# Optimization experiments

Measured on AMD Instinct MI355X. Metric: run time of the kernel, lower is better.

Reference implementation:

```python
import jax, jax.numpy as jnp
import numpy as np

B, S, H, Q = 32, 128, 128, 3  # users, seq_len, hidden_size, quadkey_level
L = Q - 1  # number of mixing scales


def setup_inputs() -> dict:
    key = jax.random.key(0)
    ks = jax.random.split(key, 12)
    trend0 = jax.random.normal(ks[0], (B, S, H), dtype=jnp.float32)
    trend1 = jax.random.normal(ks[1], (B, S, H), dtype=jnp.float32)
    trend2 = jax.random.normal(ks[2], (B, S, H), dtype=jnp.float32)
    # Per-position prefix linears padded into dense tensors, zero-masked beyond
    # the prefix length j+1 so the ragged math is exact:
    #   W1[j, :j+1, :j+1] ~ Linear(j+1, j+1), b1[j, :j+1]
    #   W2[j, :j+1]      ~ Linear(j+1, 1),   b2[j]
    idx = jnp.arange(S)
    pm = (idx[None, :] <= idx[:, None]).astype(jnp.float32)  # [j, s]: s <= j
    W1 = jax.random.normal(ks[3], (L, S, S, S), dtype=jnp.float32) * 0.05
    W1 = W1 * pm[None, :, :, None] * pm[None, :, None, :]
    b1 = jax.random.normal(ks[4], (L, S, S), dtype=jnp.float32) * 0.05 * pm[None]
    W2 = jax.random.normal(ks[5], (L, S, S), dtype=jnp.float32) * 0.05 * pm[None]
    b2 = jax.random.normal(ks[6], (L, S), dtype=jnp.float32) * 0.05
    # shared output MLP: Linear(H,H)->GELU->Linear(H,H); stored as [in, out]
    Wm1 = jax.random.normal(ks[7], (H, H), dtype=jnp.float32) * 0.05
    bm1 = jax.random.normal(ks[8], (H,), dtype=jnp.float32) * 0.05
    Wm2 = jax.random.normal(ks[9], (H, H), dtype=jnp.float32) * 0.05
    bm2 = jax.random.normal(ks[10], (H,), dtype=jnp.float32) * 0.05
    return {"trend0": trend0, "trend1": trend1, "trend2": trend2,
            "W1": W1, "b1": b1, "W2": W2, "b2": b2,
            "Wm1": Wm1, "bm1": bm1, "Wm2": Wm2, "bm2": bm2}


def reference(trend0, trend1, trend2, W1, b1, W2, b2, Wm1, bm1, Wm2, bm2):
    gelu = lambda x: jax.nn.gelu(x, approximate=False)  # torch nn.GELU default
    mlp = lambda x: gelu(x @ Wm1 + bm1) @ Wm2 + bm2

    rev = [trend2, trend1, trend0]  # trend_list reversed
    out_low = rev[0]
    out_high = rev[1]
    outs = [out_low]
    for i in range(Q - 1):
        # vectorized ragged prefix mix: per position j, out_low[:, :j+1] (as [B,H,j+1])
        # -> Linear(j+1,j+1) -> GELU -> Linear(j+1,1). Zero-padding in W1/b1/W2
        # kills all contributions beyond the prefix (GELU(0)=0).
        y1 = jnp.einsum('bsh,jst->bhjt', out_low, W1[i]) + b1[i]  # [B,H,S,S]
        res = jnp.einsum('bhjt,jt->bjh', gelu(y1), W2[i]) + b2[i][None, :, None]
        out_high = out_high + res
        out_low = out_high
        if i + 2 <= Q - 1:
            out_high = rev[i + 2]
        out_low = mlp(out_low)
        outs.append(out_low)
    outs.reverse()
    return tuple(outs)
```

## Files before the change

### kernel.cpp

```cpp
#include <hip/hip_runtime.h>
#include <stdint.h>

#define BSH (32 * 128 * 128)

typedef __attribute__((ext_vector_type(8))) __bf16 bf16x8;
typedef __attribute__((ext_vector_type(4))) float f32x4;

__device__ __forceinline__ unsigned short f2bf(float f) {
  union { float f; unsigned u; } v; v.f = f;
  return (unsigned short)((v.u + 0x7FFFu + ((v.u >> 16) & 1u)) >> 16);
}

__device__ __forceinline__ float fast_exp2(float x) {
#if __has_builtin(__builtin_amdgcn_exp2f)
  return __builtin_amdgcn_exp2f(x);
#else
  float r; asm("v_exp_f32 %0, %1" : "=v"(r) : "v"(x)); return r;
#endif
}
__device__ __forceinline__ float fast_rcp(float x) {
#if __has_builtin(__builtin_amdgcn_rcpf)
  return __builtin_amdgcn_rcpf(x);
#else
  float r; asm("v_rcp_f32 %0, %1" : "=v"(r) : "v"(x)); return r;
#endif
}

__device__ __forceinline__ float gelu_f(float y) {
  float u = y * y;
  float p = __builtin_fmaf(u, 0.044715f, 1.0f) * y;
  float w = fast_exp2(p * 2.30220787f);
  return y - y * fast_rcp(1.0f + w);
}

__device__ __forceinline__ int jg_of(int x, int cls) {
  return cls == 0 ? x : cls == 1 ? 15 - x : cls == 2 ? 16 + x : 31 - x;
}

__device__ __forceinline__ void transpose_block_c(const float* __restrict__ src,
                                                  unsigned short* __restrict__ dst,
                                                  unsigned short* lds) {
  const int tid = threadIdx.x;
  const float4* s4 = (const float4*)src;
#pragma unroll
  for (int it = 0; it < 16; ++it) {
    int i4 = tid + it * 256;
    float4 v = s4[i4];
    int s = i4 >> 5;
    int t0 = (i4 * 4) & 127;
    int sc = s >> 3, se = s & 7;
#pragma unroll
    for (int e = 0; e < 4; ++e) {
      int t = t0 + e;
      lds[t * 136 + ((sc ^ ((t >> 2) & 7)) << 3) + se] = f2bf(((const float*)&v)[e]);
    }
  }
  __syncthreads();
#pragma unroll
  for (int it = 0; it < 8; ++it) {
    int c = tid + it * 256;
    int tr = c >> 4, sc = c & 15;
    uint4 d = *(const uint4*)(lds + tr * 136 + ((sc ^ ((tr >> 2) & 7)) << 3));
    *(uint4*)(dst + (sc * 128 + tr) * 8) = d;
  }
}

__global__ __launch_bounds__(256) void prepass_kernel(
    const float* __restrict__ W1, const float* __restrict__ trend2,
    const float* __restrict__ Wm1, const float* __restrict__ Wm2,
    unsigned short* __restrict__ W1Tc, unsigned short* __restrict__ T2c,
    unsigned short* __restrict__ Wm1c, unsigned short* __restrict__ Wm2c,
    float* __restrict__ out2) {
  __shared__ unsigned short lds[128 * 136];
  const int bid = blockIdx.x;
  if (bid < 256) {
    int x = bid & 7, r = bid >> 3;
    int stage = r >> 4, rr = r & 15;
    int j = jg_of(x, rr >> 2) * 4 + (rr & 3);
    int blk = stage * 128 + j;
    transpose_block_c(W1 + blk * 16384, W1Tc + blk * 16384, lds);
  } else if (bid < 288) {
    const int b = bid - 256;
    transpose_block_c(trend2 + b * 16384, T2c + b * 16384, lds);
    const float4* s4 = (const float4*)(trend2 + b * 16384);
    float4* d4 = (float4*)(out2 + b * 16384);
#pragma unroll
    for (int it = 0; it < 16; ++it)
      d4[threadIdx.x + it * 256] = s4[threadIdx.x + it * 256];
  } else if (bid == 288) {
    transpose_block_c(Wm1, Wm1c, lds);
  } else {
    transpose_block_c(Wm2, Wm2c, lds);
  }
}

__global__ __launch_bounds__(256, 4) void mix_fused_kernel(
    const unsigned short* __restrict__ XTc,
    const unsigned short* __restrict__ W1Tj,
    const float* __restrict__ b1j,
    const float* __restrict__ W2j,
    const float* __restrict__ b2j,
    const float* __restrict__ trendR,
    const unsigned short* __restrict__ Wm1c,
    const unsigned short* __restrict__ Wm2c,
    const float* __restrict__ bm1,
    const float* __restrict__ bm2,
    float* __restrict__ outF,
    unsigned short* __restrict__ outTc,
    const int write_t) {
  __shared__ float res_ws[4][4][64];
  __shared__ __align__(16) unsigned short xa[16 * 128];
  __shared__ __align__(16) unsigned short U[16 * 128];
  const int bid = blockIdx.x;
  const int x = bid & 7;
  const int i = bid >> 3;
  const int b = i & 31;
  const int jg = jg_of(x, i >> 5);
  const int j0 = jg * 4;
  const int tid = threadIdx.x;
  const int wave = tid >> 6;
  const int lane = tid & 63;
  const int lane15 = lane & 15;
  const int quad = lane >> 4;

  {
    uint4 z = {0, 0, 0, 0};
    ((uint4*)xa)[tid] = z;
    ((uint4*)U)[tid] = z;
  }

  const int ntiles = (j0 >> 4) + 1;
  const int ksteps = (j0 >> 5) + 1;
  const unsigned short* Bb = XTc + b * 16384;
  const unsigned short* A0 = W1Tj + j0 * 16384;
  const float C = -2.45546937f;

#pragma unroll
  for (int p = 0; p < 2; ++p) {
    float psum[4][4];
#pragma unroll
    for (int jj = 0; jj < 4; ++jj)
#pragma unroll
      for (int ni = 0; ni < 4; ++ni) psum[jj][ni] = 0.f;

#pragma unroll
    for (int q = 0; q < 2; ++q) {
      const int mt = wave + q * 4;
      if (mt < ntiles) {
        f32x4 acc[4][4];
#pragma unroll
        for (int jj = 0; jj < 4; ++jj)
#pragma unroll
          for (int ni = 0; ni < 4; ++ni) {
            f32x4 z = {0.f, 0.f, 0.f, 0.f};
            acc[jj][ni] = z;
          }
        for (int ks = 0; ks < ksteps; ++ks) {
          const int kq = ks * 4 + quad;
          const unsigned short* bp = Bb + (kq * 128 + p * 64 + lane15) * 8;
          bf16x8 bfr[4], af[4];
#pragma unroll
          for (int ni = 0; ni < 4; ++ni)
            bfr[ni] = *(const bf16x8*)(bp + ni * 128);
#pragma unroll
          for (int jj = 0; jj < 4; ++jj)
            af[jj] = *(const bf16x8*)(A0 + jj * 16384 +
                                      (kq * 128 + mt * 16 + lane15) * 8);
#pragma unroll
          for (int jj = 0; jj < 4; ++jj)
#pragma unroll
            for (int ni = 0; ni < 4; ++ni)
              acc[jj][ni] = __builtin_amdgcn_mfma_f32_16x16x32_bf16(
                  af[jj], bfr[ni], acc[jj][ni], 0, 0, 0);
        }
        const int tb = mt * 16 + quad * 4;
#pragma unroll
        for (int jj = 0; jj < 4; ++jj) {
          const int j = j0 + jj;
          float4 b1v = *(const float4*)(b1j + j * 128 + tb);
          float4 w2v = *(const float4*)(W2j + j * 128 + tb);
#pragma unroll
          for (int r = 0; r < 4; ++r) {
            float b1r = ((const float*)&b1v)[r];
            float w2r = ((const float*)&w2v)[r];
            float cb = C * b1r;
            float bw = b1r * w2r;
#pragma unroll
            for (int ni = 0; ni < 4; ++ni) {
              float a = acc[jj][ni][r];
              float m = __builtin_fmaf(a, C, cb);
              float e = fast_exp2(m);
              float rr2 = fast_rcp(1.0f + e);
              float yw = __builtin_fmaf(a, w2r, bw);
              psum[jj][ni] = __builtin_fmaf(yw, rr2, psum[jj][ni]);
            }
          }
        }
      }
    }
#pragma unroll
    for (int jj = 0; jj < 4; ++jj)
#pragma unroll
      for (int ni = 0; ni < 4; ++ni) {
        float v = psum[jj][ni];
        v += __shfl_xor(v, 16, 64);
        v += __shfl_xor(v, 32, 64);
        psum[jj][ni] = v;
      }
#pragma unroll
    for (int jj = 0; jj < 4; ++jj)
      res_ws[wave][jj][quad * 16 + lane15] = psum[jj][quad];
    __syncthreads();
    {
      const int jj = tid >> 6;
      const int hh = tid & 63;
      const int j = j0 + jj;
      const int h = p * 64 + hh;
      float v = res_ws[0][jj][hh] + res_ws[1][jj][hh] +
                res_ws[2][jj][hh] + res_ws[3][jj][hh] +
                b2j[j] + trendR[(b * 128 + j) * 128 + h];
      xa[((h >> 3) * 16 + jj) * 8 + (h & 7)] = f2bf(v);
    }
    __syncthreads();
  }

  f32x4 acc2[2];
  { f32x4 z = {0.f, 0.f, 0.f, 0.f}; acc2[0] = z; acc2[1] = z; }
#pragma unroll
  for (int ks = 0; ks < 4; ++ks) {
    int kq = ks * 4 + quad;
    bf16x8 a = *(const bf16x8*)(xa + (kq * 16 + lane15) * 8);
    bf16x8 w0 = *(const bf16x8*)(Wm1c + (kq * 128 + (wave * 2 + 0) * 16 + lane15) * 8);
    bf16x8 w1 = *(const bf16x8*)(Wm1c + (kq * 128 + (wave * 2 + 1) * 16 + lane15) * 8);
    acc2[0] = __builtin_amdgcn_mfma_f32_16x16x32_bf16(a, w0, acc2[0], 0, 0, 0);
    acc2[1] = __builtin_amdgcn_mfma_f32_16x16x32_bf16(a, w1, acc2[1], 0, 0, 0);
  }
  if (quad == 0) {
#pragma unroll
    for (int nt = 0; nt < 2; ++nt) {
      int o = (wave * 2 + nt) * 16 + lane15;
      float bv = bm1[o];
#pragma unroll
      for (int r = 0; r < 4; ++r) {
        float g = gelu_f(acc2[nt][r] + bv);
        U[((o >> 3) * 16 + r) * 8 + (o & 7)] = f2bf(g);
      }
    }
  }
  __syncthreads();
  { f32x4 z = {0.f, 0.f, 0.f, 0.f}; acc2[0] = z; acc2[1] = z; }
#pragma unroll
  for (int ks = 0; ks < 4; ++ks) {
    int kq = ks * 4 + quad;
    bf16x8 a = *(const bf16x8*)(U + (kq * 16 + lane15) * 8);
    bf16x8 w0 = *(const bf16x8*)(Wm2c + (kq * 128 + (wave * 2 + 0) * 16 + lane15) * 8);
    bf16x8 w1 = *(const bf16x8*)(Wm2c + (kq * 128 + (wave * 2 + 1) * 16 + lane15) * 8);
    acc2[0] = __builtin_amdgcn_mfma_f32_16x16x32_bf16(a, w0, acc2[0], 0, 0, 0);
    acc2[1] = __builtin_amdgcn_mfma_f32_16x16x32_bf16(a, w1, acc2[1], 0, 0, 0);
  }
  if (quad == 0) {
#pragma unroll
    for (int nt = 0; nt < 2; ++nt) {
      int o = (wave * 2 + nt) * 16 + lane15;
      float bv = bm2[o];
      unsigned short tmp4[4] __attribute__((aligned(8)));
#pragma unroll
      for (int r = 0; r < 4; ++r) {
        float v = acc2[nt][r] + bv;
        outF[b * 16384 + (j0 + r) * 128 + o] = v;
        tmp4[r] = f2bf(v);
      }
      if (write_t)
        *(uint2*)(outTc + b * 16384 + ((j0 >> 3) * 128 + o) * 8 + (j0 & 7)) =
            *(const uint2*)tmp4;
    }
  }
}

extern "C" void kernel_launch(void* const* d_in, const int* in_sizes, int n_in,
                              void* d_out, int out_size, void* d_ws, size_t ws_size,
                              hipStream_t stream) {
  (void)in_sizes; (void)n_in; (void)out_size; (void)ws_size;
  const float* trend0 = (const float*)d_in[0];
  const float* trend1 = (const float*)d_in[1];
  const float* trend2 = (const float*)d_in[2];
  const float* W1  = (const float*)d_in[3];
  const float* b1  = (const float*)d_in[4];
  const float* W2  = (const float*)d_in[5];
  const float* b2  = (const float*)d_in[6];
  const float* Wm1 = (const float*)d_in[7];
  const float* bm1 = (const float*)d_in[8];
  const float* Wm2 = (const float*)d_in[9];
  const float* bm2 = (const float*)d_in[10];
  float* out = (float*)d_out;
  char* ws = (char*)d_ws;

  unsigned short* W1Tc = (unsigned short*)(ws);
  unsigned short* T2c  = (unsigned short*)(ws + 8388608);
  unsigned short* A1Tc = (unsigned short*)(ws + 9437184);
  unsigned short* Wm1c = (unsigned short*)(ws + 10485760);
  unsigned short* Wm2c = (unsigned short*)(ws + 10518528);

  prepass_kernel<<<290, 256, 0, stream>>>(W1, trend2, Wm1, Wm2,
                                          W1Tc, T2c, Wm1c, Wm2c, out + 2 * BSH);
  mix_fused_kernel<<<1024, 256, 0, stream>>>(
      T2c, W1Tc, b1, W2, b2, trend1, Wm1c, Wm2c, bm1, bm2,
      out + BSH, A1Tc, 1);
  mix_fused_kernel<<<1024, 256, 0, stream>>>(
      A1Tc, W1Tc + 128 * 16384, b1 + 16384, W2 + 16384, b2 + 128, trend0,
      Wm1c, Wm2c, bm1, bm2, out, (unsigned short*)nullptr, 0);
}
```

Measured before the change: 145.8 us.

## Split j-tile accumulation into pairs and software-pipeline fragment loads

The MFMA accumulation loop now handles two j-rows at a time instead of four, which halves the accumulator registers live at once. Each k-step prefetches the next step's A and B fragments before issuing the current MFMAs, so global/L2 load latency can overlap with matrix math. The cost is that the B fragments are loaded twice per q-tile, once for each j-pair, which raises load traffic. Lower register pressure may allow higher occupancy.

```diff
diff --git a/kernel.cpp b/kernel.cpp
--- a/kernel.cpp
+++ b/kernel.cpp
@@ -147,52 +147,74 @@
     for (int q = 0; q < 2; ++q) {
       const int mt = wave + q * 4;
       if (mt < ntiles) {
-        f32x4 acc[4][4];
-#pragma unroll
-        for (int jj = 0; jj < 4; ++jj)
-#pragma unroll
-          for (int ni = 0; ni < 4; ++ni) {
-            f32x4 z = {0.f, 0.f, 0.f, 0.f};
-            acc[jj][ni] = z;
+        const unsigned short* bp0 = Bb + (p * 64 + lane15) * 8;
+        const unsigned short* ap0 = A0 + (mt * 16 + lane15) * 8;
+        const int tb = mt * 16 + quad * 4;
+#pragma unroll
+        for (int pr = 0; pr < 2; ++pr) {
+          const unsigned short* aP = ap0 + (pr * 2) * 16384;
+          f32x4 acc[2][4];
+#pragma unroll
+          for (int jl = 0; jl < 2; ++jl)
+#pragma unroll
+            for (int ni = 0; ni < 4; ++ni) {
+              f32x4 z = {0.f, 0.f, 0.f, 0.f};
+              acc[jl][ni] = z;
+            }
+          int kq = quad;
+          bf16x8 ac0 = *(const bf16x8*)(aP + kq * 1024);
+          bf16x8 ac1 = *(const bf16x8*)(aP + 16384 + kq * 1024);
+          bf16x8 bc0 = *(const bf16x8*)(bp0 + kq * 1024);
+          bf16x8 bc1 = *(const bf16x8*)(bp0 + kq * 1024 + 128);
+          bf16x8 bc2 = *(const bf16x8*)(bp0 + kq * 1024 + 256);
+          bf16x8 bc3 = *(const bf16x8*)(bp0 + kq * 1024 + 384);
+          for (int ks = 0;;) {
+            const bool more = (ks + 1 < ksteps);
+            bf16x8 an0, an1, bn0, bn1, bn2, bn3;
+            if (more) {
+              const int k2 = kq + 4;
+              an0 = *(const bf16x8*)(aP + k2 * 1024);
+              an1 = *(const bf16x8*)(aP + 16384 + k2 * 1024);
+              bn0 = *(const bf16x8*)(bp0 + k2 * 1024);
+              bn1 = *(const bf16x8*)(bp0 + k2 * 1024 + 128);
+              bn2 = *(const bf16x8*)(bp0 + k2 * 1024 + 256);
+              bn3 = *(const bf16x8*)(bp0 + k2 * 1024 + 384);
+            }
+            acc[0][0] = __builtin_amdgcn_mfma_f32_16x16x32_bf16(ac0, bc0, acc[0][0], 0, 0, 0);
+            acc[1][0] = __builtin_amdgcn_mfma_f32_16x16x32_bf16(ac1, bc0, acc[1][0], 0, 0, 0);
+            acc[0][1] = __builtin_amdgcn_mfma_f32_16x16x32_bf16(ac0, bc1, acc[0][1], 0, 0, 0);
+            acc[1][1] = __builtin_amdgcn_mfma_f32_16x16x32_bf16(ac1, bc1, acc[1][1], 0, 0, 0);
+            acc[0][2] = __builtin_amdgcn_mfma_f32_16x16x32_bf16(ac0, bc2, acc[0][2], 0, 0, 0);
+            acc[1][2] = __builtin_amdgcn_mfma_f32_16x16x32_bf16(ac1, bc2, acc[1][2], 0, 0, 0);
+            acc[0][3] = __builtin_amdgcn_mfma_f32_16x16x32_bf16(ac0, bc3, acc[0][3], 0, 0, 0);
+            acc[1][3] = __builtin_amdgcn_mfma_f32_16x16x32_bf16(ac1, bc3, acc[1][3], 0, 0, 0);
+            ++ks;
+            if (!more) break;
+            kq += 4;
+            ac0 = an0; ac1 = an1;
+            bc0 = bn0; bc1 = bn1; bc2 = bn2; bc3 = bn3;
           }
-        for (int ks = 0; ks < ksteps; ++ks) {
-          const int kq = ks * 4 + quad;
-          const unsigned short* bp = Bb + (kq * 128 + p * 64 + lane15) * 8;
-          bf16x8 bfr[4], af[4];
-#pragma unroll
-          for (int ni = 0; ni < 4; ++ni)
-            bfr[ni] = *(const bf16x8*)(bp + ni * 128);
-#pragma unroll
-          for (int jj = 0; jj < 4; ++jj)
-            af[jj] = *(const bf16x8*)(A0 + jj * 16384 +
-                                      (kq * 128 + mt * 16 + lane15) * 8);
-#pragma unroll
-          for (int jj = 0; jj < 4; ++jj)
-#pragma unroll
-            for (int ni = 0; ni < 4; ++ni)
-              acc[jj][ni] = __builtin_amdgcn_mfma_f32_16x16x32_bf16(
-                  af[jj], bfr[ni], acc[jj][ni], 0, 0, 0);
-        }
-        const int tb = mt * 16 + quad * 4;
-#pragma unroll
-        for (int jj = 0; jj < 4; ++jj) {
-          const int j = j0 + jj;
-          float4 b1v = *(const float4*)(b1j + j * 128 + tb);
-          float4 w2v = *(const float4*)(W2j + j * 128 + tb);
-#pragma unroll
-          for (int r = 0; r < 4; ++r) {
-            float b1r = ((const float*)&b1v)[r];
-            float w2r = ((const float*)&w2v)[r];
-            float cb = C * b1r;
-            float bw = b1r * w2r;
-#pragma unroll
-            for (int ni = 0; ni < 4; ++ni) {
-              float a = acc[jj][ni][r];
-              float m = __builtin_fmaf(a, C, cb);
-              float e = fast_exp2(m);
-              float rr2 = fast_rcp(1.0f + e);
-              float yw = __builtin_fmaf(a, w2r, bw);
-              psum[jj][ni] = __builtin_fmaf(yw, rr2, psum[jj][ni]);
+#pragma unroll
+          for (int jl = 0; jl < 2; ++jl) {
+            const int jj = pr * 2 + jl;
+            const int j = j0 + jj;
+            float4 b1v = *(const float4*)(b1j + j * 128 + tb);
+            float4 w2v = *(const float4*)(W2j + j * 128 + tb);
+#pragma unroll
+            for (int r = 0; r < 4; ++r) {
+              float b1r = ((const float*)&b1v)[r];
+              float w2r = ((const float*)&w2v)[r];
+              float cb = C * b1r;
+              float bw = b1r * w2r;
+#pragma unroll
+              for (int ni = 0; ni < 4; ++ni) {
+                float a = acc[jl][ni][r];
+                float m = __builtin_fmaf(a, C, cb);
+                float e = fast_exp2(m);
+                float rr2 = fast_rcp(1.0f + e);
+                float yw = __builtin_fmaf(a, w2r, bw);
+                psum[jj][ni] = __builtin_fmaf(yw, rr2, psum[jj][ni]);
+              }
             }
           }
         }
```

Measured after the change: 201.8 us. 1.38x slower.
